# Optimization experiments

Measured on AMD Instinct MI355X. Metric: run time of the kernel, lower is better.

## Reference

```python
import jax, jax.numpy as jnp
from jax import lax
import numpy as np

# --- config (torchvision Mask R-CNN RPN / RoIAlign defaults) ---
IMG = 800.0        # image size (square)
STRIDE = 4.0       # FPN level stride -> feature 200x200
K_PRE = 2000       # pre-NMS top-k proposals
K_POST = 512       # post-NMS proposals kept
IOU_THR = 0.7      # RPN NMS IoU threshold
OUT = 7            # RoIAlign output size
SR = 2             # RoIAlign sampling ratio
SCALE = 1.0 / STRIDE
BBOX_XFORM_CLIP = 4.135166556742356  # log(1000/16)


def setup_inputs() -> dict:
    key = jax.random.key(0)
    k1, k2, k3 = jax.random.split(key, 3)
    C, H, W = 256, 200, 200
    feature = jax.random.normal(k1, (C, H, W), jnp.float32)
    # anchor grid: 3 sizes per location, stride 4 (proper geometric anchors)
    sizes = np.array([32.0, 64.0, 128.0], np.float32)
    ys, xs = np.meshgrid(np.arange(H, dtype=np.float32) * STRIDE,
                         np.arange(W, dtype=np.float32) * STRIDE, indexing='ij')
    ctr = np.stack([xs, ys], axis=-1).reshape(-1, 1, 2)            # [HW,1,2] (x,y)
    half = np.stack([sizes / 2, sizes / 2], axis=-1)[None]          # [1,3,2]
    anchors = np.concatenate([ctr - half + 0 * half, ctr + half], axis=-1)
    anchors = np.broadcast_to(np.concatenate([ctr - half, ctr + half], -1),
                              (H * W, 3, 4)).reshape(-1, 4).astype(np.float32)
    N = anchors.shape[0]  # 120000
    objectness = jax.random.normal(k2, (N,), jnp.float32)
    deltas = jax.random.normal(k3, (N, 4), jnp.float32) * 0.1
    return {"feature": feature, "objectness": objectness,
            "deltas": deltas, "anchors": jnp.asarray(anchors)}


def decode_boxes(deltas, anchors):
    w = anchors[:, 2] - anchors[:, 0]
    h = anchors[:, 3] - anchors[:, 1]
    cx = anchors[:, 0] + 0.5 * w
    cy = anchors[:, 1] + 0.5 * h
    dx, dy = deltas[:, 0], deltas[:, 1]
    dw = jnp.minimum(deltas[:, 2], BBOX_XFORM_CLIP)
    dh = jnp.minimum(deltas[:, 3], BBOX_XFORM_CLIP)
    pcx = dx * w + cx
    pcy = dy * h + cy
    pw = jnp.exp(dw) * w
    ph = jnp.exp(dh) * h
    boxes = jnp.stack([pcx - 0.5 * pw, pcy - 0.5 * ph,
                       pcx + 0.5 * pw, pcy + 0.5 * ph], axis=-1)
    return jnp.clip(boxes, 0.0, IMG)


def pairwise_iou(b):  # b: [K,4]
    area = (b[:, 2] - b[:, 0]) * (b[:, 3] - b[:, 1])
    lt = jnp.maximum(b[:, None, :2], b[None, :, :2])
    rb = jnp.minimum(b[:, None, 2:], b[None, :, 2:])
    wh = jnp.maximum(rb - lt, 0.0)
    inter = wh[..., 0] * wh[..., 1]
    return inter / (area[:, None] + area[None, :] - inter + 1e-6)


def nms_suppress(boxes_sorted, iou_thr):
    # boxes sorted by descending score; returns keep mask [K]
    K = boxes_sorted.shape[0]
    iou = pairwise_iou(boxes_sorted)
    js = jnp.arange(K)
    def body(i, supp):
        row = (iou[i] > iou_thr) & (js > i)
        return jnp.where(supp[i], supp, supp | row)
    supp = lax.fori_loop(0, K, body, jnp.zeros((K,), bool))
    return ~supp


def roi_align(feature, boxes):
    # feature: [C,H,W]; boxes: [M,4] in image coords; aligned=False variant
    C, H, W = feature.shape
    P = OUT * SR
    def one(box):
        x1, y1, x2, y2 = box[0] * SCALE, box[1] * SCALE, box[2] * SCALE, box[3] * SCALE
        rw = jnp.maximum(x2 - x1, 1.0)
        rh = jnp.maximum(y2 - y1, 1.0)
        idx = jnp.arange(P, dtype=feature.dtype) + 0.5
        ys = y1 + idx * (rh / P)   # [P]
        xs = x1 + idx * (rw / P)
        yy, xx = jnp.meshgrid(ys, xs, indexing='ij')     # [P,P]
        y = jnp.clip(yy, 0.0, H - 1.0)
        x = jnp.clip(xx, 0.0, W - 1.0)
        y0 = jnp.floor(y).astype(jnp.int32)
        x0 = jnp.floor(x).astype(jnp.int32)
        y1i = jnp.minimum(y0 + 1, H - 1)
        x1i = jnp.minimum(x0 + 1, W - 1)
        ly = y - y0.astype(feature.dtype)
        lx = x - x0.astype(feature.dtype)
        v00 = feature[:, y0, x0]    # [C,P,P]
        v01 = feature[:, y0, x1i]
        v10 = feature[:, y1i, x0]
        v11 = feature[:, y1i, x1i]
        val = (v00 * (1 - ly) * (1 - lx) + v01 * (1 - ly) * lx
               + v10 * ly * (1 - lx) + v11 * ly * lx)  # [C,P,P]
        return val.reshape(C, OUT, SR, OUT, SR).mean(axis=(2, 4))  # [C,7,7]
    return jax.vmap(one)(boxes)


def reference(feature, objectness, deltas, anchors):
    boxes = decode_boxes(deltas, anchors)                    # [N,4]
    scores, idx = lax.top_k(objectness, K_PRE)               # pre-NMS top-k
    cand = boxes[idx]                                        # [K_PRE,4] sorted
    keep = nms_suppress(cand, IOU_THR)                       # [K_PRE] bool
    masked = jnp.where(keep, scores, -jnp.inf)
    _, fidx = lax.top_k(masked, K_POST)                      # post-NMS top-k
    final_boxes = cand[fidx]                                 # [K_POST,4]
    valid = keep[fidx].astype(feature.dtype)                 # [K_POST]
    roi = roi_align(feature, final_boxes)                    # [K_POST,256,7,7]
    return roi * valid[:, None, None, None]
```

## Files before the change

### kernel.cpp

```cpp
#include <hip/hip_runtime.h>
#include <cstdint>
#include <cstddef>

#define N_ANCH   120000
#define K_PRE    2000
#define K_POST   512
#define CAP      4096
#define NWORD    32
#define HBINS    4096
#define IOU_THR  0.7f
#define IMGF     800.0f
#define CLIPV    4.135166556742356f
#define FH       200
#define FW       200
#define FC       256
#define SCALE    0.25f

#define TROWS    96
#define NTILE    21
#define CH       8

#define CG       32
#define TPE      4

typedef unsigned long long u64;
typedef float f2u __attribute__((ext_vector_type(2), aligned(4)));

struct Ws {
    uint32_t T;
    uint32_t cnt;
    int32_t  nk;
    uint32_t pad;
    u64      combo[CAP];
    float4   cand[K_PRE];
    int      rows[K_POST];
    u64      mask[(size_t)K_PRE * NWORD];
};

__device__ inline uint32_t fkey(float f) {
    uint32_t u = __float_as_uint(f);
    return (u & 0x80000000u) ? ~u : (u | 0x80000000u);
}

__global__ __launch_bounds__(1024) void zero_k(Ws* __restrict__ ws) {
    uint32_t* h = (uint32_t*)ws->mask;
    for (int i = threadIdx.x; i < HBINS; i += 1024) h[i] = 0u;
    if (threadIdx.x == 0) { ws->cnt = 0u; ws->nk = 0; ws->T = 0u; }
}

__global__ __launch_bounds__(256) void hist_k(const float* __restrict__ obj,
                                              uint32_t* __restrict__ hist) {
    __shared__ uint32_t h[HBINS];
    for (int i = threadIdx.x; i < HBINS; i += 256) h[i] = 0u;
    __syncthreads();
    const float4* o4 = (const float4*)obj;
    for (int i = blockIdx.x * 256 + threadIdx.x; i < N_ANCH / 4; i += gridDim.x * 256) {
        float4 v = o4[i];
        atomicAdd(&h[fkey(v.x) >> 20], 1u);
        atomicAdd(&h[fkey(v.y) >> 20], 1u);
        atomicAdd(&h[fkey(v.z) >> 20], 1u);
        atomicAdd(&h[fkey(v.w) >> 20], 1u);
    }
    __syncthreads();
    for (int i = threadIdx.x; i < HBINS; i += 256)
        if (h[i]) atomicAdd(&hist[i], h[i]);
}

__global__ __launch_bounds__(256) void gather_k(const float* __restrict__ obj,
                                                const uint32_t* __restrict__ hist,
                                                Ws* __restrict__ ws) {
    __shared__ uint32_t wsum[4];
    __shared__ uint32_t sT;
    const int tid = threadIdx.x;
    const int lane = tid & 63, wave = tid >> 6;
    uint32_t c[16]; uint32_t s = 0;
#pragma unroll
    for (int k = 0; k < 16; ++k) { c[k] = hist[HBINS - 1 - (16 * tid + k)]; s += c[k]; }
    uint32_t incl = s;
    for (int off = 1; off < 64; off <<= 1) {
        uint32_t t = __shfl_up(incl, off);
        if (lane >= off) incl += t;
    }
    if (lane == 63) wsum[wave] = incl;
    __syncthreads();
    uint32_t wpre = 0;
    for (int w2 = 0; w2 < wave; ++w2) wpre += wsum[w2];
    uint32_t before = wpre + incl - s;
#pragma unroll
    for (int k = 0; k < 16; ++k) {
        uint32_t after = before + c[k];
        if (before < K_PRE && after >= K_PRE)
            sT = (uint32_t)(HBINS - 1 - (16 * tid + k)) << 20;
        before = after;
    }
    __syncthreads();
    const uint32_t T = sT;
    int i = blockIdx.x * 256 + tid;
    if (i >= N_ANCH / 4) return;
    float4 v = ((const float4*)obj)[i];
    float vals[4] = {v.x, v.y, v.z, v.w};
#pragma unroll
    for (int k = 0; k < 4; ++k) {
        uint32_t u = fkey(vals[k]);
        if (u >= T) {
            uint32_t pos = atomicAdd(&ws->cnt, 1u);
            if (pos < CAP)
                ws->combo[pos] = ((u64)(~u) << 32) | (uint32_t)(4 * i + k);
        }
    }
}

__global__ __launch_bounds__(256) void rank_decode_k(const float* __restrict__ deltas,
                                                     const float* __restrict__ anchors,
                                                     Ws* __restrict__ ws) {
    __shared__ u64 sc[CAP];
    const int tid = threadIdx.x;
    int M = (int)ws->cnt;
    if (M > CAP) M = CAP;
    const int ebase = blockIdx.x * (256 / TPE);
    if (ebase >= M) return;
    for (int e = tid; e < M; e += 256) sc[e] = ws->combo[e];
    __syncthreads();
    const int gid = ebase + tid / TPE;
    const int sub = tid & (TPE - 1);
    if (gid >= M) return;
    const u64 mine = sc[gid];
    int cnt = 0;
    int j = sub;
    for (; j + 3 * TPE < M; j += 4 * TPE) {
        u64 a = sc[j], b = sc[j + TPE], c = sc[j + 2 * TPE], d = sc[j + 3 * TPE];
        cnt += (int)(a < mine) + (int)(b < mine) + (int)(c < mine) + (int)(d < mine);
    }
    for (; j < M; j += TPE) cnt += (int)(sc[j] < mine);
    cnt += __shfl_xor(cnt, 1);
    cnt += __shfl_xor(cnt, 2);
    if (sub == 0 && cnt < K_PRE) {
        const uint32_t idx = (uint32_t)(mine & 0xFFFFFFFFull);
        float a0 = anchors[idx * 4 + 0], a1 = anchors[idx * 4 + 1];
        float a2 = anchors[idx * 4 + 2], a3 = anchors[idx * 4 + 3];
        float d0 = deltas[idx * 4 + 0],  d1 = deltas[idx * 4 + 1];
        float d2 = fminf(deltas[idx * 4 + 2], CLIPV);
        float d3 = fminf(deltas[idx * 4 + 3], CLIPV);
        float w = a2 - a0, h = a3 - a1;
        float cx = a0 + 0.5f * w, cy = a1 + 0.5f * h;
        float pcx = d0 * w + cx, pcy = d1 * h + cy;
        float pw = expf(d2) * w, ph = expf(d3) * h;
        float x1 = fminf(fmaxf(pcx - 0.5f * pw, 0.0f), IMGF);
        float y1 = fminf(fmaxf(pcy - 0.5f * ph, 0.0f), IMGF);
        float x2 = fminf(fmaxf(pcx + 0.5f * pw, 0.0f), IMGF);
        float y2 = fminf(fmaxf(pcy + 0.5f * ph, 0.0f), IMGF);
        ws->cand[cnt] = make_float4(x1, y1, x2, y2);
    }
}

__global__ __launch_bounds__(256) void nms_mask_k(Ws* __restrict__ ws) {
    const int i = blockIdx.x;
    const int lane = threadIdx.x & 63;
    const int wave = threadIdx.x >> 6;
    const float4 bi = ws->cand[i];
    const float ai = (bi.z - bi.x) * (bi.w - bi.y);
    for (int wd = wave; wd < NWORD; wd += 4) {
        int j = wd * 64 + lane;
        bool bit = false;
        if (j < K_PRE && j > i) {
            float4 bj = ws->cand[j];
            float aj = (bj.z - bj.x) * (bj.w - bj.y);
            float xx1 = fmaxf(bi.x, bj.x);
            float yy1 = fmaxf(bi.y, bj.y);
            float xx2 = fminf(bi.z, bj.z);
            float yy2 = fminf(bi.w, bj.w);
            float ww = fmaxf(xx2 - xx1, 0.0f);
            float hh = fmaxf(yy2 - yy1, 0.0f);
            float inter = ww * hh;
            float iou = inter / (ai + aj - inter + 1e-6f);
            bit = iou > IOU_THR;
        }
        u64 bal = __ballot(bit);
        if (lane == 0) ws->mask[(size_t)i * NWORD + wd] = bal;
    }
}

__global__ __launch_bounds__(512) void nms_scan_k(Ws* __restrict__ ws) {
    __shared__ __align__(16) u64 sbuf[2][TROWS * NWORD];
    __shared__ int s_stop;
    const int tid = threadIdx.x;
    const int lane = tid & 63;
    const int wave = tid >> 6;
    const int lmod = lane & 31;
    const u64* __restrict__ mask = ws->mask;

    {
        const ulonglong2* src = (const ulonglong2*)mask;
        ulonglong2* dst = (ulonglong2*)sbuf[0];
        for (int e = tid; e < TROWS * NWORD / 2; e += 512) dst[e] = src[e];
    }
    if (tid == 0) s_stop = 0;
    __syncthreads();

    u64 supp = 0ull;
    int kcnt = 0;
    int decided = 0;
    for (int t = 0; t < NTILE; ++t) {
        const int base = t * TROWS;
        const int nb = min(TROWS, K_PRE - base);
        if (wave == 0) {
            const u64* sm = sbuf[t & 1];
            u64 A[CH], B[CH];
#pragma unroll
            for (int b = 0; b < CH; ++b) A[b] = sm[b * NWORD + lmod];
            for (int s = 0; s < nb; s += 2 * CH) {
                const bool hasB = (s + CH) < nb;
                if (hasB) {
#pragma unroll
                    for (int b = 0; b < CH; ++b) B[b] = sm[(s + CH + b) * NWORD + lmod];
                }
                {
                    const int w = (base + s) >> 6;
                    const int bofs = (base + s) & 63;
                    u64 keptw = 0ull;
                    if (lane == w) {
                        u64 cur = supp;
#pragma unroll
                        for (int b = 0; b < CH; ++b) {
                            u64 bit = (cur >> (bofs + b)) & 1ull;
                            u64 sel = bit - 1ull;
                            cur |= A[b] & sel;
                            keptw |= sel & (1ull << b);
                        }
                        supp = cur;
                    }
                    u64 kb = __shfl(keptw, w);
                    kcnt += __popcll(kb);
#pragma unroll
                    for (int b = 0; b < CH; ++b) {
                        u64 sel = 0ull - ((kb >> b) & 1ull);
                        supp |= A[b] & sel;
                    }
                }
                if (hasB) {
                    if (s + 2 * CH < nb) {
#pragma unroll
                        for (int b = 0; b < CH; ++b)
                            A[b] = sm[(s + 2 * CH + b) * NWORD + lmod];
                    }
                    const int w = (base + s + CH) >> 6;
                    const int bofs = (base + s + CH) & 63;
                    u64 keptw = 0ull;
                    if (lane == w) {
                        u64 cur = supp;
#pragma unroll
                        for (int b = 0; b < CH; ++b) {
                            u64 bit = (cur >> (bofs + b)) & 1ull;
                            u64 sel = bit - 1ull;
                            cur |= B[b] & sel;
                            keptw |= sel & (1ull << b);
                        }
                        supp = cur;
                    }
                    u64 kb = __shfl(keptw, w);
                    kcnt += __popcll(kb);
#pragma unroll
                    for (int b = 0; b < CH; ++b) {
                        u64 sel = 0ull - ((kb >> b) & 1ull);
                        supp |= B[b] & sel;
                    }
                }
            }
            decided = base + nb;
            if (lane == 0 && kcnt >= K_POST) s_stop = 1;
        } else if (t + 1 < NTILE) {
            const int nbase = (t + 1) * TROWS;
            const int npairs = (min(TROWS, K_PRE - nbase) * NWORD) / 2;
            const ulonglong2* src = (const ulonglong2*)(mask + (size_t)nbase * NWORD);
            ulonglong2* dst = (ulonglong2*)sbuf[(t + 1) & 1];
            for (int e = tid - 64; e < npairs; e += 448) dst[e] = src[e];
        }
        __syncthreads();
        if (s_stop) break;
    }

    if (wave == 0) {
        u64 valid;
        if (lane < NWORD - 1)       valid = ~0ull;
        else if (lane == NWORD - 1) valid = (1ull << (K_PRE - (NWORD - 1) * 64)) - 1ull;
        else                        valid = 0ull;
        const int dw = decided - lane * 64;
        const u64 dmask = (dw <= 0) ? 0ull : ((dw >= 64) ? ~0ull : ((1ull << dw) - 1ull));
        u64 keepw = (~supp) & valid & dmask;
        int cnt = __popcll(keepw);
        int incl = cnt;
        for (int off = 1; off < 64; off <<= 1) {
            int t = __shfl_up(incl, off);
            if (lane >= off) incl += t;
        }
        int pos = incl - cnt;
        u64 kw = keepw;
        while (kw) {
            int b = __ffsll((unsigned long long)kw) - 1;
            kw &= kw - 1ull;
            if (pos < K_POST) ws->rows[pos] = lane * 64 + b;
            ++pos;
        }
        int total = __shfl(incl, 63);
        if (lane == 0) ws->nk = total;
        int start = total < K_POST ? total : K_POST;
        for (int r = start + lane; r < K_POST; r += 64) ws->rows[r] = -1;
    }
}

__global__ __launch_bounds__(256) void roi_k(const float* __restrict__ feat,
                                             const Ws* __restrict__ ws,
                                             float* __restrict__ out) {
    const int g = blockIdx.x;
    const int q = g & 7;
    const int r = g >> 3;
    const int cbase = q * CG;
    float* oblk = out + (size_t)r * (FC * 49) + (size_t)cbase * 49;
    const int row = ws->rows[r];
    const int tid = threadIdx.x;

    if (row < 0) {
        for (int e = tid; e < CG * 49; e += 256) oblk[e] = 0.0f;
        return;
    }
    if (tid >= 245) return;

    const int p = tid % 49;
    const int cslot = tid / 49;
    const int oy = p / 7, ox = p % 7;

    const float4 bx = ws->cand[row];
    const float x1 = bx.x * SCALE, y1 = bx.y * SCALE;
    const float x2 = bx.z * SCALE, y2 = bx.w * SCALE;
    const float rw = fmaxf(x2 - x1, 1.0f);
    const float rh = fmaxf(y2 - y1, 1.0f);
    const float stepx = rw / 14.0f;
    const float stepy = rh / 14.0f;

    int    off0[4], off1[4];
    float4 w4[4];
#pragma unroll
    for (int sub = 0; sub < 4; ++sub) {
        const int sy = sub >> 1, sx = sub & 1;
        float yy = y1 + ((float)(2 * oy + sy) + 0.5f) * stepy;
        float y = fminf(fmaxf(yy, 0.0f), (float)(FH - 1));
        float fy0 = floorf(y);
        int iy0 = (int)fy0;
        int iy1 = min(iy0 + 1, FH - 1);
        float ly = y - fy0;
        float xx = x1 + ((float)(2 * ox + sx) + 0.5f) * stepx;
        float x = fminf(fmaxf(xx, 0.0f), (float)(FW - 1));
        float fx0 = floorf(x);
        int ix0 = (int)fx0;
        float lx = x - fx0;
        float wxl, wxr; int base;
        if (ix0 >= FW - 1) { base = FW - 2; wxl = 0.0f; wxr = 1.0f; }
        else               { base = ix0;    wxl = 1.0f - lx; wxr = lx; }
        float wy0 = 1.0f - ly, wy1 = ly;
        off0[sub] = iy0 * FW + base;
        off1[sub] = iy1 * FW + base;
        w4[sub] = make_float4(wy0 * wxl * 0.25f, wy0 * wxr * 0.25f,
                              wy1 * wxl * 0.25f, wy1 * wxr * 0.25f);
    }

#pragma unroll
    for (int m = 0; m < 4; ++m) {
        const int c0 = cslot + 10 * m;
        const int c1 = c0 + 5;
        const bool v0 = c0 < CG;
        const bool v1 = c1 < CG;
        const float* f0 = feat + (size_t)(cbase + (v0 ? c0 : 0)) * (FH * FW);
        const float* f1 = feat + (size_t)(cbase + (v1 ? c1 : 0)) * (FH * FW);
        f2u r0[8], r1[8];
#pragma unroll
        for (int sub = 0; sub < 4; ++sub) {
            r0[2 * sub]     = *(const f2u*)(f0 + off0[sub]);
            r0[2 * sub + 1] = *(const f2u*)(f0 + off1[sub]);
            r1[2 * sub]     = *(const f2u*)(f1 + off0[sub]);
            r1[2 * sub + 1] = *(const f2u*)(f1 + off1[sub]);
        }
        float a0 = 0.0f, a1 = 0.0f;
#pragma unroll
        for (int sub = 0; sub < 4; ++sub) {
            a0 += w4[sub].x * r0[2 * sub].x + w4[sub].y * r0[2 * sub].y
                + w4[sub].z * r0[2 * sub + 1].x + w4[sub].w * r0[2 * sub + 1].y;
            a1 += w4[sub].x * r1[2 * sub].x + w4[sub].y * r1[2 * sub].y
                + w4[sub].z * r1[2 * sub + 1].x + w4[sub].w * r1[2 * sub + 1].y;
        }
        if (v0) oblk[c0 * 49 + p] = a0;
        if (v1) oblk[c1 * 49 + p] = a1;
    }
}

extern "C" void kernel_launch(void* const* d_in, const int* in_sizes, int n_in,
                              void* d_out, int out_size, void* d_ws, size_t ws_size,
                              hipStream_t stream) {
    const float* feature    = (const float*)d_in[0];
    const float* objectness = (const float*)d_in[1];
    const float* deltas     = (const float*)d_in[2];
    const float* anchors    = (const float*)d_in[3];
    Ws* ws = (Ws*)d_ws;
    uint32_t* hist = (uint32_t*)ws->mask;
    float* out = (float*)d_out;

    hipLaunchKernelGGL(zero_k, dim3(1), dim3(1024), 0, stream, ws);
    hipLaunchKernelGGL(hist_k, dim3(256), dim3(256), 0, stream, objectness, hist);
    hipLaunchKernelGGL(gather_k, dim3((N_ANCH / 4 + 255) / 256), dim3(256), 0, stream,
                       objectness, hist, ws);
    hipLaunchKernelGGL(rank_decode_k, dim3(CAP / (256 / TPE)), dim3(256), 0, stream,
                       deltas, anchors, ws);
    hipLaunchKernelGGL(nms_mask_k, dim3(K_PRE), dim3(256), 0, stream, ws);
    hipLaunchKernelGGL(nms_scan_k, dim3(1), dim3(512), 0, stream, ws);
    hipLaunchKernelGGL(roi_k, dim3(8 * K_POST), dim3(256), 0, stream, feature, ws, out);
}
```

Baseline: 208.9 us.

## Split RoIAlign channel groups to 16 and map blocks so each XCD handles fixed channel slices

Halves the channels per RoIAlign block from 32 to 16 and doubles the grid to 8192 blocks. Block indices are remapped so the low three bits (the XCD under round-robin dispatch) together with the upper half select the channel group. Each XCD then reads only two fixed feature-channel slices, which should improve L2 locality. The inner loop is rewritten as a 10+5+1 channel schedule with no loop or predicates. In exchange, each block recomputes the sampling offsets for fewer channels and a single wave does the 16th channel alone, leaving the others idle.

```diff
diff --git a/kernel.cpp b/kernel.cpp
--- a/kernel.cpp
+++ b/kernel.cpp
@@ -20,7 +20,7 @@
 #define NTILE    21
 #define CH       8
 
-#define CG       32
+#define CG       16
 #define TPE      4
 
 typedef unsigned long long u64;
@@ -311,10 +311,12 @@
 __global__ __launch_bounds__(256) void roi_k(const float* __restrict__ feat,
                                              const Ws* __restrict__ ws,
                                              float* __restrict__ out) {
-    const int g = blockIdx.x;
-    const int q = g & 7;
-    const int r = g >> 3;
-    const int cbase = q * CG;
+    const int b = blockIdx.x;
+    const int xcd = b & 7;
+    const int s = b >> 3;
+    const int r = s & (K_POST - 1);
+    const int cg = xcd + 8 * (s >> 9);
+    const int cbase = cg * CG;
     float* oblk = out + (size_t)r * (FC * 49) + (size_t)cbase * 49;
     const int row = ws->rows[r];
     const int tid = threadIdx.x;
@@ -363,14 +365,11 @@
                               wy1 * wxl * 0.25f, wy1 * wxr * 0.25f);
     }
 
-#pragma unroll
-    for (int m = 0; m < 4; ++m) {
-        const int c0 = cslot + 10 * m;
-        const int c1 = c0 + 5;
-        const bool v0 = c0 < CG;
-        const bool v1 = c1 < CG;
-        const float* f0 = feat + (size_t)(cbase + (v0 ? c0 : 0)) * (FH * FW);
-        const float* f1 = feat + (size_t)(cbase + (v1 ? c1 : 0)) * (FH * FW);
+    {
+        const int c0 = cslot;
+        const int c1 = cslot + 5;
+        const float* f0 = feat + (size_t)(cbase + c0) * (FH * FW);
+        const float* f1 = feat + (size_t)(cbase + c1) * (FH * FW);
         f2u r0[8], r1[8];
 #pragma unroll
         for (int sub = 0; sub < 4; ++sub) {
@@ -387,8 +386,44 @@
             a1 += w4[sub].x * r1[2 * sub].x + w4[sub].y * r1[2 * sub].y
                 + w4[sub].z * r1[2 * sub + 1].x + w4[sub].w * r1[2 * sub + 1].y;
         }
-        if (v0) oblk[c0 * 49 + p] = a0;
-        if (v1) oblk[c1 * 49 + p] = a1;
+        oblk[c0 * 49 + p] = a0;
+        oblk[c1 * 49 + p] = a1;
+    }
+
+    {
+        const int c2 = cslot + 10;
+        const float* f2 = feat + (size_t)(cbase + c2) * (FH * FW);
+        f2u r2[8];
+#pragma unroll
+        for (int sub = 0; sub < 4; ++sub) {
+            r2[2 * sub]     = *(const f2u*)(f2 + off0[sub]);
+            r2[2 * sub + 1] = *(const f2u*)(f2 + off1[sub]);
+        }
+        float a2 = 0.0f;
+#pragma unroll
+        for (int sub = 0; sub < 4; ++sub) {
+            a2 += w4[sub].x * r2[2 * sub].x + w4[sub].y * r2[2 * sub].y
+                + w4[sub].z * r2[2 * sub + 1].x + w4[sub].w * r2[2 * sub + 1].y;
+        }
+        oblk[c2 * 49 + p] = a2;
+
+        if (cslot == 0) {
+            const int c3 = 15;
+            const float* f3 = feat + (size_t)(cbase + c3) * (FH * FW);
+            f2u r3[8];
+#pragma unroll
+            for (int sub = 0; sub < 4; ++sub) {
+                r3[2 * sub]     = *(const f2u*)(f3 + off0[sub]);
+                r3[2 * sub + 1] = *(const f2u*)(f3 + off1[sub]);
+            }
+            float a3 = 0.0f;
+#pragma unroll
+            for (int sub = 0; sub < 4; ++sub) {
+                a3 += w4[sub].x * r3[2 * sub].x + w4[sub].y * r3[2 * sub].y
+                    + w4[sub].z * r3[2 * sub + 1].x + w4[sub].w * r3[2 * sub + 1].y;
+            }
+            oblk[c3 * 49 + p] = a3;
+        }
     }
 }
 
@@ -411,5 +446,5 @@
                        deltas, anchors, ws);
     hipLaunchKernelGGL(nms_mask_k, dim3(K_PRE), dim3(256), 0, stream, ws);
     hipLaunchKernelGGL(nms_scan_k, dim3(1), dim3(512), 0, stream, ws);
-    hipLaunchKernelGGL(roi_k, dim3(8 * K_POST), dim3(256), 0, stream, feature, ws, out);
-}
+    hipLaunchKernelGGL(roi_k, dim3(16 * K_POST), dim3(256), 0, stream, feature, ws, out);
+}
```

Result: faster. 199.5 us (-4.5%).
